# Kernel optimization log

Hardware: AMD Instinct MI355X
Metric: run time of the kernel (lower is better)

## Reference

```python
import jax, jax.numpy as jnp
import numpy as np

N, E = 50000, 800000
NFEAT, HID, NHEAD, NCLASS = 256, 32, 8, 40
NEG_SLOPE = 0.2


def gat_conv(x, src, dst, W, a_src, a_dst, bias, heads, out_ch, concat):
    n = x.shape[0]
    h = (x @ W).reshape(n, heads, out_ch)              # [N, H, C]
    alpha_src = jnp.einsum('nhc,hc->nh', h, a_src)     # [N, H]
    alpha_dst = jnp.einsum('nhc,hc->nh', h, a_dst)
    e = jax.nn.leaky_relu(alpha_src[src] + alpha_dst[dst], NEG_SLOPE)  # [E, H]
    # segment softmax over incoming edges of each dst node
    m = jax.ops.segment_max(e, dst, num_segments=n)
    ex = jnp.exp(e - m[dst])
    s = jax.ops.segment_sum(ex, dst, num_segments=n)
    alpha = ex / (s[dst] + 1e-16)                      # [E, H]
    out = jax.ops.segment_sum(h[src] * alpha[:, :, None], dst, num_segments=n)  # [N, H, C]
    out = out.reshape(n, heads * out_ch) if concat else out.mean(axis=1)
    return out + bias


def setup_inputs() -> dict:
    key = jax.random.key(0)
    ks = jax.random.split(key, 12)
    x = jax.random.normal(ks[0], (N, NFEAT), dtype=jnp.float32)
    edge_index = jax.random.randint(ks[1], (2, E), 0, N, dtype=jnp.int64)
    edge_attr = jax.random.normal(ks[2], (E, 8), dtype=jnp.float32)  # unused by the model
    s1 = 1.0 / np.sqrt(NFEAT)
    s2 = 1.0 / np.sqrt(HID * NHEAD)
    W1 = jax.random.normal(ks[3], (NFEAT, NHEAD * HID), dtype=jnp.float32) * s1
    att_src1 = jax.random.normal(ks[4], (NHEAD, HID), dtype=jnp.float32) * 0.1
    att_dst1 = jax.random.normal(ks[5], (NHEAD, HID), dtype=jnp.float32) * 0.1
    b1 = jnp.zeros((NHEAD * HID,), dtype=jnp.float32)
    W2 = jax.random.normal(ks[6], (NHEAD * HID, NCLASS), dtype=jnp.float32) * s2
    att_src2 = jax.random.normal(ks[7], (1, NCLASS), dtype=jnp.float32) * 0.1
    att_dst2 = jax.random.normal(ks[8], (1, NCLASS), dtype=jnp.float32) * 0.1
    b2 = jnp.zeros((NCLASS,), dtype=jnp.float32)
    return {"x": x, "edge_index": edge_index, "edge_attr": edge_attr,
            "W1": W1, "att_src1": att_src1, "att_dst1": att_dst1, "b1": b1,
            "W2": W2, "att_src2": att_src2, "att_dst2": att_dst2, "b2": b2}


def reference(x, edge_index, edge_attr, W1, att_src1, att_dst1, b1, W2, att_src2, att_dst2, b2):
    # eval mode: dropout is identity. GATConv adds self-loops by default.
    n = x.shape[0]
    loops = jnp.arange(n, dtype=edge_index.dtype)
    src = jnp.concatenate([edge_index[0], loops])
    dst = jnp.concatenate([edge_index[1], loops])
    h = jax.nn.elu(gat_conv(x, src, dst, W1, att_src1, att_dst1, b1, NHEAD, HID, True))
    final = gat_conv(h, src, dst, W2, att_src2, att_dst2, b2, 1, NCLASS, False)
    return final, jax.nn.log_softmax(final, axis=1)
```

## Files before the change

### kernel.cpp

```cpp
#include <hip/hip_runtime.h>
#include <hip/hip_bf16.h>
#include <hip/hip_fp16.h>
#include <math.h>

#define NN 50000
#define EE 800000
#define ET 850000
#define F1 256
#define NHEAD 8
#define HID 32
#define NCLASS 40
#define NEG 0.2f

typedef __attribute__((ext_vector_type(8))) short short8_t;
typedef __attribute__((ext_vector_type(4))) float float4_t;

__device__ __forceinline__ int clampN(int v) {
    return v < 0 ? 0 : (v >= NN ? NN - 1 : v);
}
__device__ __forceinline__ unsigned short f2bf(float f) {
    __hip_bfloat16 h = __float2bfloat16(f);
    return __builtin_bit_cast(unsigned short, h);
}
__device__ __forceinline__ float bf2f(unsigned short u) {
    return __uint_as_float((unsigned)u << 16);
}
__device__ __forceinline__ unsigned short f2h(float f) {
    __half h = __float2half(f);
    return __builtin_bit_cast(unsigned short, h);
}
__device__ __forceinline__ float h2f(unsigned short u) {
    __half h = __builtin_bit_cast(__half, u);
    return __half2float(h);
}
__device__ __forceinline__ float hlo2f(unsigned int u) {
    return h2f((unsigned short)(u & 0xFFFFu));
}
__device__ __forceinline__ float hhi2f(unsigned int u) {
    return h2f((unsigned short)(u >> 16));
}

__global__ __launch_bounds__(256) void hist_kernel(const int* __restrict__ ei, int* __restrict__ deg,
                                                   unsigned int* __restrict__ pack) {
    int t = blockIdx.x * 256 + threadIdx.x;
    if (t >= ET) return;
    int d = (t < EE) ? ei[EE + t] : (t - EE);
    d = clampN(d);
    int r = atomicAdd(&deg[d], 1);
    pack[t] = ((unsigned)d << 15) | (unsigned)r;
}

__global__ __launch_bounds__(256) void scan1_kernel(const int* __restrict__ deg, int* __restrict__ off, int* __restrict__ bsum) {
    __shared__ int lds[256];
    int b = blockIdx.x, tid = threadIdx.x;
    int base = b * 1024 + tid * 4;
    int v0 = (base + 0 < NN) ? deg[base + 0] : 0;
    int v1 = (base + 1 < NN) ? deg[base + 1] : 0;
    int v2 = (base + 2 < NN) ? deg[base + 2] : 0;
    int v3 = (base + 3 < NN) ? deg[base + 3] : 0;
    int s1 = v0 + v1, s2 = s1 + v2, s3 = s2 + v3;
    lds[tid] = s3;
    __syncthreads();
    for (int o = 1; o < 256; o <<= 1) {
        int t = (tid >= o) ? lds[tid - o] : 0;
        __syncthreads();
        if (tid >= o) lds[tid] += t;
        __syncthreads();
    }
    int excl = tid ? lds[tid - 1] : 0;
    if (base + 0 < NN) off[base + 1] = excl + v0;
    if (base + 1 < NN) off[base + 2] = excl + s1;
    if (base + 2 < NN) off[base + 3] = excl + s2;
    if (base + 3 < NN) off[base + 4] = excl + s3;
    if (tid == 255) bsum[b] = lds[255];
}

__global__ __launch_bounds__(256) void scan2_kernel(int* __restrict__ bsum, int nb) {
    __shared__ int lds[256];
    int tid = threadIdx.x;
    lds[tid] = (tid < nb) ? bsum[tid] : 0;
    __syncthreads();
    for (int o = 1; o < 256; o <<= 1) {
        int t = (tid >= o) ? lds[tid - o] : 0;
        __syncthreads();
        if (tid >= o) lds[tid] += t;
        __syncthreads();
    }
    if (tid < nb) bsum[tid] = lds[tid];
}

__global__ __launch_bounds__(256) void scan3_kernel(int* __restrict__ off, const int* __restrict__ bsum) {
    int b = blockIdx.x, tid = threadIdx.x;
    if (b == 0 && tid == 0) off[0] = 0;
    if (b == 0) return;
    int add = bsum[b - 1];
    int base = b * 1024 + tid * 4;
    #pragma unroll
    for (int i = 0; i < 4; ++i) {
        if (base + i < NN) off[base + i + 1] += add;
    }
}

__global__ __launch_bounds__(256) void scatter_kernel(const int* __restrict__ ei, const int* __restrict__ off,
                                                      const unsigned int* __restrict__ pack, int* __restrict__ esrc) {
    int t = blockIdx.x * 256 + threadIdx.x;
    if (t >= ET) return;
    unsigned p = pack[t];
    int d = p >> 15;
    int r = p & 0x7FFF;
    int s = (t < EE) ? ei[t] : (t - EE);
    s = clampN(s);
    esrc[off[d] + r] = s;
}

__global__ __launch_bounds__(256) void prep_kernel(const float* __restrict__ W1,
                                                   const float* __restrict__ as1, const float* __restrict__ ad1,
                                                   unsigned short* __restrict__ Bh, unsigned short* __restrict__ Bl) {
    int n = blockIdx.x;
    int k = threadIdx.x;
    float v;
    if (n < 256) {
        v = W1[(size_t)k * 256 + n];
    } else {
        int j = n - 256;
        int h = j & 7;
        const float* att = (j < 8) ? (as1 + h * 32) : (ad1 + h * 32);
        float s = 0.f;
        #pragma unroll
        for (int c = 0; c < 32; ++c) s += W1[(size_t)k * 256 + h * 32 + c] * att[c];
        v = s;
    }
    unsigned short hi = f2bf(v);
    Bh[n * 256 + k] = hi;
    Bl[n * 256 + k] = f2bf(v - bf2f(hi));
}

#define AKP 40
__global__ __launch_bounds__(256, 2) void gemm1_kernel(const float* __restrict__ x,
                                                       const unsigned short* __restrict__ Bh,
                                                       const unsigned short* __restrict__ Bl,
                                                       unsigned short* __restrict__ h1b,
                                                       float* __restrict__ asrc1, float* __restrict__ adst1) {
    __shared__ __align__(16) unsigned short Ah[128 * AKP];
    __shared__ __align__(16) unsigned short Al[128 * AKP];
    __shared__ __align__(16) unsigned short Bhs[272 * AKP];
    __shared__ __align__(16) unsigned short Bls[272 * AKP];
    int tid = threadIdx.x;
    int wave = tid >> 6, lane = tid & 63;
    int quad = lane >> 4, l16 = lane & 15;
    int row0 = blockIdx.x * 128;

    float4_t acc[2][17];
    #pragma unroll
    for (int i = 0; i < 2; ++i)
        #pragma unroll
        for (int j = 0; j < 17; ++j) acc[i][j] = (float4_t){0.f, 0.f, 0.f, 0.f};

    for (int k0 = 0; k0 < 256; k0 += 32) {
        __syncthreads();
        #pragma unroll
        for (int i = 0; i < 4; ++i) {
            int id = i * 256 + tid;
            int r = id >> 3, kq = id & 7;
            int rr = row0 + r; if (rr >= NN) rr = NN - 1;
            float4 v = *(const float4*)(x + (size_t)rr * 256 + k0 + kq * 4);
            ushort4 hi, lo;
            hi.x = f2bf(v.x); lo.x = f2bf(v.x - bf2f(hi.x));
            hi.y = f2bf(v.y); lo.y = f2bf(v.y - bf2f(hi.y));
            hi.z = f2bf(v.z); lo.z = f2bf(v.z - bf2f(hi.z));
            hi.w = f2bf(v.w); lo.w = f2bf(v.w - bf2f(hi.w));
            *(ushort4*)(Ah + r * AKP + kq * 4) = hi;
            *(ushort4*)(Al + r * AKP + kq * 4) = lo;
        }
        for (int id = tid; id < 272 * 4; id += 256) {
            int r = id >> 2, kq = id & 3;
            *(float4*)(Bhs + r * AKP + kq * 8) = *(const float4*)(Bh + (size_t)r * 256 + k0 + kq * 8);
            *(float4*)(Bls + r * AKP + kq * 8) = *(const float4*)(Bl + (size_t)r * 256 + k0 + kq * 8);
        }
        __syncthreads();
        short8_t ah[2], al[2];
        #pragma unroll
        for (int mt = 0; mt < 2; ++mt) {
            int mrow = wave * 32 + mt * 16 + l16;
            ah[mt] = *(const short8_t*)(Ah + mrow * AKP + quad * 8);
            al[mt] = *(const short8_t*)(Al + mrow * AKP + quad * 8);
        }
        #pragma unroll
        for (int nt = 0; nt < 17; ++nt) {
            int nrow = nt * 16 + l16;
            short8_t bh  = *(const short8_t*)(Bhs + nrow * AKP + quad * 8);
            short8_t blo = *(const short8_t*)(Bls + nrow * AKP + quad * 8);
            #pragma unroll
            for (int mt = 0; mt < 2; ++mt) {
                acc[mt][nt] = __builtin_amdgcn_mfma_f32_16x16x32_bf16(ah[mt], bh,  acc[mt][nt], 0, 0, 0);
                acc[mt][nt] = __builtin_amdgcn_mfma_f32_16x16x32_bf16(ah[mt], blo, acc[mt][nt], 0, 0, 0);
                acc[mt][nt] = __builtin_amdgcn_mfma_f32_16x16x32_bf16(al[mt], bh,  acc[mt][nt], 0, 0, 0);
            }
        }
    }
    #pragma unroll
    for (int mt = 0; mt < 2; ++mt) {
        int rbase = row0 + wave * 32 + mt * 16 + quad * 4;
        #pragma unroll
        for (int r = 0; r < 4; ++r) {
            int row = rbase + r;
            if (row >= NN) continue;
            #pragma unroll
            for (int nt = 0; nt < 16; ++nt)
                h1b[(size_t)row * 256 + nt * 16 + l16] = f2h(acc[mt][nt][r]);
            float v = acc[mt][16][r];
            if (l16 < 8) asrc1[row * 8 + l16] = v;
            else         adst1[row * 8 + (l16 - 8)] = v;
        }
    }
}

#define WST 68
__global__ __launch_bounds__(256) void agg1_kernel(const unsigned short* __restrict__ h1b, const float* __restrict__ asrc,
                                                   const float* __restrict__ adst, const int* __restrict__ esrc,
                                                   const int* __restrict__ off,
                                                   const float* __restrict__ b1, unsigned short* __restrict__ hout) {
    __shared__ __align__(16) float wl[4][8 * WST];
    __shared__ __align__(16) int  snl[4][64];
    int tid = threadIdx.x;
    int wave = tid >> 6;
    int wid = blockIdx.x * 4 + wave;
    if (wid >= NN) return;
    int lane = tid & 63;
    int hp = lane & 7;
    int jp = lane >> 3;
    int hc = lane >> 3;
    int c0 = lane * 4;
    float adh_p = adst[wid * 8 + hp];
    int e0 = off[wid], e1 = off[wid + 1];
    float* wlw = wl[wave];
    int* snw = snl[wave];
    const char* hb = (const char*)h1b;
    unsigned lofs = (unsigned)c0 * 2;

    float m = -INFINITY, s = 0.f;
    float ax = 0.f, ay = 0.f, az = 0.f, aw = 0.f;

    for (int base = e0; base < e1; base += 64) {
        int cnt = e1 - base; if (cnt > 64) cnt = 64;
        int snv = esrc[base + (lane < cnt ? lane : cnt - 1)];
        snw[lane] = snv;
        int nch = (cnt + 7) >> 3;
        float ee[8];
        float wmax = -INFINITY;
        #pragma unroll
        for (int cj = 0; cj < 8; ++cj) {
            if (cj >= nch) { ee[cj] = -INFINITY; continue; }
            int jedge = cj * 8 + jp;
            int sj = __shfl(snv, jedge);
            float a = asrc[sj * 8 + hp];
            float e = a + adh_p;
            e = (e >= 0.f) ? e : NEG * e;
            if (jedge >= cnt) e = -INFINITY;
            ee[cj] = e;
            wmax = fmaxf(wmax, e);
        }
        wmax = fmaxf(wmax, __shfl_xor(wmax, 8));
        wmax = fmaxf(wmax, __shfl_xor(wmax, 16));
        wmax = fmaxf(wmax, __shfl_xor(wmax, 32));
        float mn = fmaxf(m, wmax);
        float t = __expf(m - mn);
        m = mn;
        s *= t;
        float tc = __shfl(t, hc);
        ax *= tc; ay *= tc; az *= tc; aw *= tc;
        #pragma unroll
        for (int cj = 0; cj < 8; ++cj) {
            if (cj >= nch) break;
            float w = __expf(ee[cj] - mn);
            s += w;
            wlw[hp * WST + cj * 8 + jp] = w;
        }
        const float* wrow = wlw + hc * WST;
        for (int j = 0; j < cnt; j += 4) {
            float4 w4 = *(const float4*)(wrow + j);
            int4 sn4 = *(const int4*)(snw + j);
            uint2 u0 = *(const uint2*)(hb + (((unsigned)sn4.x << 9) + lofs));
            uint2 u1 = *(const uint2*)(hb + (((unsigned)sn4.y << 9) + lofs));
            uint2 u2 = *(const uint2*)(hb + (((unsigned)sn4.z << 9) + lofs));
            uint2 u3 = *(const uint2*)(hb + (((unsigned)sn4.w << 9) + lofs));
            ax += w4.x * hlo2f(u0.x);
            ay += w4.x * hhi2f(u0.x);
            az += w4.x * hlo2f(u0.y);
            aw += w4.x * hhi2f(u0.y);
            ax += w4.y * hlo2f(u1.x);
            ay += w4.y * hhi2f(u1.x);
            az += w4.y * hlo2f(u1.y);
            aw += w4.y * hhi2f(u1.y);
            ax += w4.z * hlo2f(u2.x);
            ay += w4.z * hhi2f(u2.x);
            az += w4.z * hlo2f(u2.y);
            aw += w4.z * hhi2f(u2.y);
            ax += w4.w * hlo2f(u3.x);
            ay += w4.w * hhi2f(u3.x);
            az += w4.w * hlo2f(u3.y);
            aw += w4.w * hhi2f(u3.y);
        }
    }
    s += __shfl_xor(s, 8);
    s += __shfl_xor(s, 16);
    s += __shfl_xor(s, 32);
    float sh = __shfl(s, hc);
    float inv = 1.f / (sh + 1e-16f);
    float4 b = *(const float4*)(b1 + c0);
    float vx = ax * inv + b.x, vy = ay * inv + b.y, vz = az * inv + b.z, vw = aw * inv + b.w;
    ushort4 o;
    o.x = f2h((vx > 0.f) ? vx : expm1f(vx));
    o.y = f2h((vy > 0.f) ? vy : expm1f(vy));
    o.z = f2h((vz > 0.f) ? vz : expm1f(vz));
    o.w = f2h((vw > 0.f) ? vw : expm1f(vw));
    *(ushort4*)(hout + (size_t)wid * 256 + c0) = o;
}

#define G2_TM 128
#define G2_KC 32
__global__ __launch_bounds__(256) void gemm2_kernel(const unsigned short* __restrict__ h, const float* __restrict__ W2,
                                                    const float* __restrict__ at_s, const float* __restrict__ at_d,
                                                    unsigned short* __restrict__ h2b, float* __restrict__ as2,
                                                    float* __restrict__ ad2) {
    __shared__ __align__(16) float w2s[256 * 40];
    __shared__ __align__(16) float As[G2_KC][132];
    int tid = threadIdx.x;
    for (int i = tid; i < 256 * 40; i += 256) w2s[i] = W2[i];
    int g  = tid & 7;
    int rg = tid >> 3;
    int row0 = blockIdx.x * G2_TM;
    float acc[4][5] = {};
    float ats[5], atd[5];
    #pragma unroll
    for (int j = 0; j < 5; ++j) { ats[j] = at_s[g + 8 * j]; atd[j] = at_d[g + 8 * j]; }

    for (int k0 = 0; k0 < 256; k0 += G2_KC) {
        __syncthreads();
        #pragma unroll
        for (int i = 0; i < 2; ++i) {
            int id = i * 256 + tid;
            int r  = id >> 2;
            int kq = id & 3;
            int rr = row0 + r; if (rr >= NN) rr = NN - 1;
            uint4 u = *(const uint4*)(h + (size_t)rr * 256 + k0 + kq * 8);
            As[kq * 8 + 0][r] = hlo2f(u.x);
            As[kq * 8 + 1][r] = hhi2f(u.x);
            As[kq * 8 + 2][r] = hlo2f(u.y);
            As[kq * 8 + 3][r] = hhi2f(u.y);
            As[kq * 8 + 4][r] = hlo2f(u.z);
            As[kq * 8 + 5][r] = hhi2f(u.z);
            As[kq * 8 + 6][r] = hlo2f(u.w);
            As[kq * 8 + 7][r] = hhi2f(u.w);
        }
        __syncthreads();
        #pragma unroll 4
        for (int k = 0; k < G2_KC; ++k) {
            float4 a = *(const float4*)(&As[k][rg * 4]);
            float w[5];
            #pragma unroll
            for (int j = 0; j < 5; ++j) w[j] = w2s[(k0 + k) * 40 + g + 8 * j];
            float av[4] = {a.x, a.y, a.z, a.w};
            #pragma unroll
            for (int r = 0; r < 4; ++r)
                #pragma unroll
                for (int j = 0; j < 5; ++j)
                    acc[r][j] += av[r] * w[j];
        }
    }

    #pragma unroll
    for (int r = 0; r < 4; ++r) {
        int row = row0 + rg * 4 + r;
        float ps = 0.f, pd = 0.f;
        #pragma unroll
        for (int j = 0; j < 5; ++j) {
            ps += acc[r][j] * ats[j];
            pd += acc[r][j] * atd[j];
        }
        ps += __shfl_xor(ps, 1); pd += __shfl_xor(pd, 1);
        ps += __shfl_xor(ps, 2); pd += __shfl_xor(pd, 2);
        ps += __shfl_xor(ps, 4); pd += __shfl_xor(pd, 4);
        if (row < NN) {
            #pragma unroll
            for (int j = 0; j < 5; ++j) h2b[(size_t)row * 40 + g + 8 * j] = f2h(acc[r][j]);
            if (g == 0) { as2[row] = ps; ad2[row] = pd; }
        }
    }
}

__global__ __launch_bounds__(256) void agg2_kernel(const unsigned short* __restrict__ h2b, const float* __restrict__ asrc,
                                                   const float* __restrict__ adst, const int* __restrict__ esrc,
                                                   const int* __restrict__ off,
                                                   const float* __restrict__ b2, float* __restrict__ outF,
                                                   float* __restrict__ outL) {
    __shared__ __align__(16) float wl2[4][64];
    __shared__ __align__(16) int  snl2[4][64];
    int tid = threadIdx.x;
    int wave = tid >> 6;
    int wid = blockIdx.x * 4 + wave;
    if (wid >= NN) return;
    int lane = tid & 63;
    int c = lane;
    float adh = adst[wid];
    int e0 = off[wid], e1 = off[wid + 1];
    const char* hb = (const char*)h2b + ((unsigned)(c < NCLASS ? c : 0) << 1);
    float* wlw = wl2[wave];
    int* snw = snl2[wave];

    float m = -INFINITY, s = 0.f, acc = 0.f;

    for (int base = e0; base < e1; base += 64) {
        int cnt = e1 - base; if (cnt > 64) cnt = 64;
        int snv = esrc[base + (lane < cnt ? lane : cnt - 1)];
        snw[lane] = snv;
        float a = asrc[snv];
        float e = a + adh;
        e = (e >= 0.f) ? e : NEG * e;
        if (lane >= cnt) e = -INFINITY;
        float cm = e;
        cm = fmaxf(cm, __shfl_xor(cm, 1));
        cm = fmaxf(cm, __shfl_xor(cm, 2));
        cm = fmaxf(cm, __shfl_xor(cm, 4));
        cm = fmaxf(cm, __shfl_xor(cm, 8));
        cm = fmaxf(cm, __shfl_xor(cm, 16));
        cm = fmaxf(cm, __shfl_xor(cm, 32));
        float mn = fmaxf(m, cm);
        float t = __expf(m - mn);
        float w = __expf(e - mn);
        s = s * t + w;
        m = mn;
        wlw[lane] = w;
        acc *= t;
        for (int j = 0; j < cnt; j += 4) {
            float4 w4 = *(const float4*)(wlw + j);
            int4 sn4 = *(const int4*)(snw + j);
            unsigned short v0 = *(const unsigned short*)(hb + (unsigned)sn4.x * 80);
            unsigned short v1 = *(const unsigned short*)(hb + (unsigned)sn4.y * 80);
            unsigned short v2 = *(const unsigned short*)(hb + (unsigned)sn4.z * 80);
            unsigned short v3 = *(const unsigned short*)(hb + (unsigned)sn4.w * 80);
            acc += w4.x * h2f(v0);
            acc += w4.y * h2f(v1);
            acc += w4.z * h2f(v2);
            acc += w4.w * h2f(v3);
        }
    }
    s += __shfl_xor(s, 1);
    s += __shfl_xor(s, 2);
    s += __shfl_xor(s, 4);
    s += __shfl_xor(s, 8);
    s += __shfl_xor(s, 16);
    s += __shfl_xor(s, 32);
    float inv = 1.f / (s + 1e-16f);
    float fin = (c < NCLASS) ? (acc * inv + b2[c]) : -INFINITY;
    if (c < NCLASS) outF[(size_t)wid * 40 + c] = fin;
    float mx = fin;
    for (int o = 32; o; o >>= 1) mx = fmaxf(mx, __shfl_xor(mx, o));
    float ex = (c < NCLASS) ? __expf(fin - mx) : 0.f;
    float sm = ex;
    for (int o = 32; o; o >>= 1) sm += __shfl_xor(sm, o);
    if (c < NCLASS) outL[(size_t)wid * 40 + c] = fin - mx - __logf(sm);
}

extern "C" void kernel_launch(void* const* d_in, const int* in_sizes, int n_in,
                              void* d_out, int out_size, void* d_ws, size_t ws_size,
                              hipStream_t stream) {
    const float* x   = (const float*)d_in[0];
    const int*   ei  = (const int*)d_in[1];
    const float* W1  = (const float*)d_in[3];
    const float* as1 = (const float*)d_in[4];
    const float* ad1 = (const float*)d_in[5];
    const float* b1  = (const float*)d_in[6];
    const float* W2  = (const float*)d_in[7];
    const float* as2c = (const float*)d_in[8];
    const float* ad2c = (const float*)d_in[9];
    const float* b2  = (const float*)d_in[10];

    float* outF = (float*)d_out;
    float* outL = outF + (size_t)NN * NCLASS;

    char* w = (char*)d_ws;
    auto alloc = [&](size_t bytes) {
        void* p = (void*)w;
        w += (bytes + 255) & ~(size_t)255;
        return p;
    };
    unsigned short* h1b = (unsigned short*)alloc((size_t)NN * 256 * 2);
    unsigned short* hbuf = (unsigned short*)alloc((size_t)NN * 256 * 2);
    unsigned short* h2b = (unsigned short*)alloc((size_t)NN * 40 * 2);
    float* asrc1 = (float*)alloc((size_t)NN * 8 * 4);
    float* adst1 = (float*)alloc((size_t)NN * 8 * 4);
    float* asrc2 = (float*)alloc((size_t)NN * 4);
    float* adst2 = (float*)alloc((size_t)NN * 4);
    int* deg    = (int*)alloc((size_t)NN * 4);
    int* off    = (int*)alloc((size_t)(NN + 1) * 4);
    unsigned int* pack = (unsigned int*)alloc((size_t)ET * 4);
    int* esrc   = (int*)alloc((size_t)ET * 4);
    int* bsum   = (int*)alloc(64 * 4);
    unsigned short* W1th = (unsigned short*)alloc((size_t)272 * 256 * 2);
    unsigned short* W1tl = (unsigned short*)alloc((size_t)272 * 256 * 2);

    const int NB_SCAN = (NN + 1023) / 1024;

    hipMemsetAsync(deg, 0, (size_t)NN * 4, stream);

    hist_kernel<<<(ET + 255) / 256, 256, 0, stream>>>(ei, deg, pack);
    scan1_kernel<<<NB_SCAN, 256, 0, stream>>>(deg, off, bsum);
    scan2_kernel<<<1, 256, 0, stream>>>(bsum, NB_SCAN);
    scan3_kernel<<<NB_SCAN, 256, 0, stream>>>(off, bsum);
    scatter_kernel<<<(ET + 255) / 256, 256, 0, stream>>>(ei, off, pack, esrc);

    prep_kernel<<<272, 256, 0, stream>>>(W1, as1, ad1, W1th, W1tl);
    gemm1_kernel<<<(NN + 127) / 128, 256, 0, stream>>>(x, W1th, W1tl, h1b, asrc1, adst1);
    agg1_kernel<<<(NN + 3) / 4, 256, 0, stream>>>(h1b, asrc1, adst1, esrc, off, b1, hbuf);
    gemm2_kernel<<<(NN + G2_TM - 1) / G2_TM, 256, 0, stream>>>(hbuf, W2, as2c, ad2c, h2b, asrc2, adst2);
    agg2_kernel<<<(NN + 3) / 4, 256, 0, stream>>>(h2b, asrc2, adst2, esrc, off, b2, outF, outL);
}
```

Before: 341.3 us.

## Use persistent grid-stride waves and scalar row addressing in GAT aggregation kernels

Both aggregation kernels now launch a fixed grid of 2048 blocks, and each wave loops over destination nodes with a grid stride instead of handling one node per wave. The gather loop is unrolled to 8 edges per step, and the source row indices are made wave-uniform with readfirstlane so addressing can use scalar registers. Edge slots are padded to multiples of 8, and the padded slots carry zero weights and repeat the last valid index. The aim is to cut launch and block-scheduling overhead and to put more loads in flight. The risk is load imbalance across waves and some wasted loads on padded edges.

Result: no change. 346.5 us (+1.5%).

```diff
diff --git a/kernel.cpp b/kernel.cpp
--- a/kernel.cpp
+++ b/kernel.cpp
@@ -224,97 +224,130 @@
     __shared__ __align__(16) int  snl[4][64];
     int tid = threadIdx.x;
     int wave = tid >> 6;
-    int wid = blockIdx.x * 4 + wave;
-    if (wid >= NN) return;
     int lane = tid & 63;
     int hp = lane & 7;
     int jp = lane >> 3;
     int hc = lane >> 3;
     int c0 = lane * 4;
-    float adh_p = adst[wid * 8 + hp];
-    int e0 = off[wid], e1 = off[wid + 1];
     float* wlw = wl[wave];
     int* snw = snl[wave];
+    const float* wrow = wlw + hc * WST;
     const char* hb = (const char*)h1b;
     unsigned lofs = (unsigned)c0 * 2;
-
-    float m = -INFINITY, s = 0.f;
-    float ax = 0.f, ay = 0.f, az = 0.f, aw = 0.f;
-
-    for (int base = e0; base < e1; base += 64) {
-        int cnt = e1 - base; if (cnt > 64) cnt = 64;
-        int snv = esrc[base + (lane < cnt ? lane : cnt - 1)];
-        snw[lane] = snv;
-        int nch = (cnt + 7) >> 3;
-        float ee[8];
-        float wmax = -INFINITY;
-        #pragma unroll
-        for (int cj = 0; cj < 8; ++cj) {
-            if (cj >= nch) { ee[cj] = -INFINITY; continue; }
-            int jedge = cj * 8 + jp;
-            int sj = __shfl(snv, jedge);
-            float a = asrc[sj * 8 + hp];
-            float e = a + adh_p;
-            e = (e >= 0.f) ? e : NEG * e;
-            if (jedge >= cnt) e = -INFINITY;
-            ee[cj] = e;
-            wmax = fmaxf(wmax, e);
-        }
-        wmax = fmaxf(wmax, __shfl_xor(wmax, 8));
-        wmax = fmaxf(wmax, __shfl_xor(wmax, 16));
-        wmax = fmaxf(wmax, __shfl_xor(wmax, 32));
-        float mn = fmaxf(m, wmax);
-        float t = __expf(m - mn);
-        m = mn;
-        s *= t;
-        float tc = __shfl(t, hc);
-        ax *= tc; ay *= tc; az *= tc; aw *= tc;
-        #pragma unroll
-        for (int cj = 0; cj < 8; ++cj) {
-            if (cj >= nch) break;
-            float w = __expf(ee[cj] - mn);
-            s += w;
-            wlw[hp * WST + cj * 8 + jp] = w;
-        }
-        const float* wrow = wlw + hc * WST;
-        for (int j = 0; j < cnt; j += 4) {
-            float4 w4 = *(const float4*)(wrow + j);
-            int4 sn4 = *(const int4*)(snw + j);
-            uint2 u0 = *(const uint2*)(hb + (((unsigned)sn4.x << 9) + lofs));
-            uint2 u1 = *(const uint2*)(hb + (((unsigned)sn4.y << 9) + lofs));
-            uint2 u2 = *(const uint2*)(hb + (((unsigned)sn4.z << 9) + lofs));
-            uint2 u3 = *(const uint2*)(hb + (((unsigned)sn4.w << 9) + lofs));
-            ax += w4.x * hlo2f(u0.x);
-            ay += w4.x * hhi2f(u0.x);
-            az += w4.x * hlo2f(u0.y);
-            aw += w4.x * hhi2f(u0.y);
-            ax += w4.y * hlo2f(u1.x);
-            ay += w4.y * hhi2f(u1.x);
-            az += w4.y * hlo2f(u1.y);
-            aw += w4.y * hhi2f(u1.y);
-            ax += w4.z * hlo2f(u2.x);
-            ay += w4.z * hhi2f(u2.x);
-            az += w4.z * hlo2f(u2.y);
-            aw += w4.z * hhi2f(u2.y);
-            ax += w4.w * hlo2f(u3.x);
-            ay += w4.w * hhi2f(u3.x);
-            az += w4.w * hlo2f(u3.y);
-            aw += w4.w * hhi2f(u3.y);
-        }
-    }
-    s += __shfl_xor(s, 8);
-    s += __shfl_xor(s, 16);
-    s += __shfl_xor(s, 32);
-    float sh = __shfl(s, hc);
-    float inv = 1.f / (sh + 1e-16f);
     float4 b = *(const float4*)(b1 + c0);
-    float vx = ax * inv + b.x, vy = ay * inv + b.y, vz = az * inv + b.z, vw = aw * inv + b.w;
-    ushort4 o;
-    o.x = f2h((vx > 0.f) ? vx : expm1f(vx));
-    o.y = f2h((vy > 0.f) ? vy : expm1f(vy));
-    o.z = f2h((vz > 0.f) ? vz : expm1f(vz));
-    o.w = f2h((vw > 0.f) ? vw : expm1f(vw));
-    *(ushort4*)(hout + (size_t)wid * 256 + c0) = o;
+    int wstride = gridDim.x * 4;
+
+    for (int wid = blockIdx.x * 4 + wave; wid < NN; wid += wstride) {
+        float adh_p = adst[wid * 8 + hp];
+        int e0 = off[wid], e1 = off[wid + 1];
+
+        float m = -INFINITY, s = 0.f;
+        float ax = 0.f, ay = 0.f, az = 0.f, aw = 0.f;
+
+        for (int base = e0; base < e1; base += 64) {
+            int cnt = e1 - base; if (cnt > 64) cnt = 64;
+            int snv = esrc[base + (lane < cnt ? lane : cnt - 1)];
+            snw[lane] = snv;
+            int nch = (cnt + 7) >> 3;
+            float ee[8];
+            float wmax = -INFINITY;
+            #pragma unroll
+            for (int cj = 0; cj < 8; ++cj) {
+                if (cj >= nch) { ee[cj] = -INFINITY; continue; }
+                int jedge = cj * 8 + jp;
+                int sj = __shfl(snv, jedge);
+                float a = asrc[sj * 8 + hp];
+                float e = a + adh_p;
+                e = (e >= 0.f) ? e : NEG * e;
+                if (jedge >= cnt) e = -INFINITY;
+                ee[cj] = e;
+                wmax = fmaxf(wmax, e);
+            }
+            wmax = fmaxf(wmax, __shfl_xor(wmax, 8));
+            wmax = fmaxf(wmax, __shfl_xor(wmax, 16));
+            wmax = fmaxf(wmax, __shfl_xor(wmax, 32));
+            float mn = fmaxf(m, wmax);
+            float t = __expf(m - mn);
+            m = mn;
+            s *= t;
+            float tc = __shfl(t, hc);
+            ax *= tc; ay *= tc; az *= tc; aw *= tc;
+            #pragma unroll
+            for (int cj = 0; cj < 8; ++cj) {
+                if (cj >= nch) break;
+                float w = __expf(ee[cj] - mn);
+                s += w;
+                wlw[hp * WST + cj * 8 + jp] = w;
+            }
+            int nslots = nch * 8;
+            for (int j = 0; j < nslots; j += 8) {
+                float4 wa = *(const float4*)(wrow + j);
+                float4 wb = *(const float4*)(wrow + j + 4);
+                int4 sa = *(const int4*)(snw + j);
+                int4 sb = *(const int4*)(snw + j + 4);
+                const char* r0 = hb + ((size_t)(unsigned)__builtin_amdgcn_readfirstlane(sa.x) << 9);
+                const char* r1 = hb + ((size_t)(unsigned)__builtin_amdgcn_readfirstlane(sa.y) << 9);
+                const char* r2 = hb + ((size_t)(unsigned)__builtin_amdgcn_readfirstlane(sa.z) << 9);
+                const char* r3 = hb + ((size_t)(unsigned)__builtin_amdgcn_readfirstlane(sa.w) << 9);
+                const char* r4 = hb + ((size_t)(unsigned)__builtin_amdgcn_readfirstlane(sb.x) << 9);
+                const char* r5 = hb + ((size_t)(unsigned)__builtin_amdgcn_readfirstlane(sb.y) << 9);
+                const char* r6 = hb + ((size_t)(unsigned)__builtin_amdgcn_readfirstlane(sb.z) << 9);
+                const char* r7 = hb + ((size_t)(unsigned)__builtin_amdgcn_readfirstlane(sb.w) << 9);
+                uint2 u0 = *(const uint2*)(r0 + lofs);
+                uint2 u1 = *(const uint2*)(r1 + lofs);
+                uint2 u2 = *(const uint2*)(r2 + lofs);
+                uint2 u3 = *(const uint2*)(r3 + lofs);
+                uint2 u4 = *(const uint2*)(r4 + lofs);
+                uint2 u5 = *(const uint2*)(r5 + lofs);
+                uint2 u6 = *(const uint2*)(r6 + lofs);
+                uint2 u7 = *(const uint2*)(r7 + lofs);
+                ax += wa.x * hlo2f(u0.x);
+                ay += wa.x * hhi2f(u0.x);
+                az += wa.x * hlo2f(u0.y);
+                aw += wa.x * hhi2f(u0.y);
+                ax += wa.y * hlo2f(u1.x);
+                ay += wa.y * hhi2f(u1.x);
+                az += wa.y * hlo2f(u1.y);
+                aw += wa.y * hhi2f(u1.y);
+                ax += wa.z * hlo2f(u2.x);
+                ay += wa.z * hhi2f(u2.x);
+                az += wa.z * hlo2f(u2.y);
+                aw += wa.z * hhi2f(u2.y);
+                ax += wa.w * hlo2f(u3.x);
+                ay += wa.w * hhi2f(u3.x);
+                az += wa.w * hlo2f(u3.y);
+                aw += wa.w * hhi2f(u3.y);
+                ax += wb.x * hlo2f(u4.x);
+                ay += wb.x * hhi2f(u4.x);
+                az += wb.x * hlo2f(u4.y);
+                aw += wb.x * hhi2f(u4.y);
+                ax += wb.y * hlo2f(u5.x);
+                ay += wb.y * hhi2f(u5.x);
+                az += wb.y * hlo2f(u5.y);
+                aw += wb.y * hhi2f(u5.y);
+                ax += wb.z * hlo2f(u6.x);
+                ay += wb.z * hhi2f(u6.x);
+                az += wb.z * hlo2f(u6.y);
+                aw += wb.z * hhi2f(u6.y);
+                ax += wb.w * hlo2f(u7.x);
+                ay += wb.w * hhi2f(u7.x);
+                az += wb.w * hlo2f(u7.y);
+                aw += wb.w * hhi2f(u7.y);
+            }
+        }
+        s += __shfl_xor(s, 8);
+        s += __shfl_xor(s, 16);
+        s += __shfl_xor(s, 32);
+        float sh = __shfl(s, hc);
+        float inv = 1.f / (sh + 1e-16f);
+        float vx = ax * inv + b.x, vy = ay * inv + b.y, vz = az * inv + b.z, vw = aw * inv + b.w;
+        ushort4 o;
+        o.x = f2h((vx > 0.f) ? vx : expm1f(vx));
+        o.y = f2h((vy > 0.f) ? vy : expm1f(vy));
+        o.z = f2h((vz > 0.f) ? vz : expm1f(vz));
+        o.w = f2h((vw > 0.f) ? vw : expm1f(vw));
+        *(ushort4*)(hout + (size_t)wid * 256 + c0) = o;
+    }
 }
 
 #define G2_TM 128
@@ -398,68 +431,91 @@
     __shared__ __align__(16) int  snl2[4][64];
     int tid = threadIdx.x;
     int wave = tid >> 6;
-    int wid = blockIdx.x * 4 + wave;
-    if (wid >= NN) return;
     int lane = tid & 63;
     int c = lane;
-    float adh = adst[wid];
-    int e0 = off[wid], e1 = off[wid + 1];
-    const char* hb = (const char*)h2b + ((unsigned)(c < NCLASS ? c : 0) << 1);
+    const char* hb = (const char*)h2b;
+    unsigned coff = (unsigned)(c < NCLASS ? c : 0) * 2;
     float* wlw = wl2[wave];
     int* snw = snl2[wave];
-
-    float m = -INFINITY, s = 0.f, acc = 0.f;
-
-    for (int base = e0; base < e1; base += 64) {
-        int cnt = e1 - base; if (cnt > 64) cnt = 64;
-        int snv = esrc[base + (lane < cnt ? lane : cnt - 1)];
-        snw[lane] = snv;
-        float a = asrc[snv];
-        float e = a + adh;
-        e = (e >= 0.f) ? e : NEG * e;
-        if (lane >= cnt) e = -INFINITY;
-        float cm = e;
-        cm = fmaxf(cm, __shfl_xor(cm, 1));
-        cm = fmaxf(cm, __shfl_xor(cm, 2));
-        cm = fmaxf(cm, __shfl_xor(cm, 4));
-        cm = fmaxf(cm, __shfl_xor(cm, 8));
-        cm = fmaxf(cm, __shfl_xor(cm, 16));
-        cm = fmaxf(cm, __shfl_xor(cm, 32));
-        float mn = fmaxf(m, cm);
-        float t = __expf(m - mn);
-        float w = __expf(e - mn);
-        s = s * t + w;
-        m = mn;
-        wlw[lane] = w;
-        acc *= t;
-        for (int j = 0; j < cnt; j += 4) {
-            float4 w4 = *(const float4*)(wlw + j);
-            int4 sn4 = *(const int4*)(snw + j);
-            unsigned short v0 = *(const unsigned short*)(hb + (unsigned)sn4.x * 80);
-            unsigned short v1 = *(const unsigned short*)(hb + (unsigned)sn4.y * 80);
-            unsigned short v2 = *(const unsigned short*)(hb + (unsigned)sn4.z * 80);
-            unsigned short v3 = *(const unsigned short*)(hb + (unsigned)sn4.w * 80);
-            acc += w4.x * h2f(v0);
-            acc += w4.y * h2f(v1);
-            acc += w4.z * h2f(v2);
-            acc += w4.w * h2f(v3);
-        }
-    }
-    s += __shfl_xor(s, 1);
-    s += __shfl_xor(s, 2);
-    s += __shfl_xor(s, 4);
-    s += __shfl_xor(s, 8);
-    s += __shfl_xor(s, 16);
-    s += __shfl_xor(s, 32);
-    float inv = 1.f / (s + 1e-16f);
-    float fin = (c < NCLASS) ? (acc * inv + b2[c]) : -INFINITY;
-    if (c < NCLASS) outF[(size_t)wid * 40 + c] = fin;
-    float mx = fin;
-    for (int o = 32; o; o >>= 1) mx = fmaxf(mx, __shfl_xor(mx, o));
-    float ex = (c < NCLASS) ? __expf(fin - mx) : 0.f;
-    float sm = ex;
-    for (int o = 32; o; o >>= 1) sm += __shfl_xor(sm, o);
-    if (c < NCLASS) outL[(size_t)wid * 40 + c] = fin - mx - __logf(sm);
+    float bc = (c < NCLASS) ? b2[c] : 0.f;
+    int wstride = gridDim.x * 4;
+
+    for (int wid = blockIdx.x * 4 + wave; wid < NN; wid += wstride) {
+        float adh = adst[wid];
+        int e0 = off[wid], e1 = off[wid + 1];
+
+        float m = -INFINITY, s = 0.f, acc = 0.f;
+
+        for (int base = e0; base < e1; base += 64) {
+            int cnt = e1 - base; if (cnt > 64) cnt = 64;
+            int snv = esrc[base + (lane < cnt ? lane : cnt - 1)];
+            snw[lane] = snv;
+            float a = asrc[snv];
+            float e = a + adh;
+            e = (e >= 0.f) ? e : NEG * e;
+            if (lane >= cnt) e = -INFINITY;
+            float cm = e;
+            cm = fmaxf(cm, __shfl_xor(cm, 1));
+            cm = fmaxf(cm, __shfl_xor(cm, 2));
+            cm = fmaxf(cm, __shfl_xor(cm, 4));
+            cm = fmaxf(cm, __shfl_xor(cm, 8));
+            cm = fmaxf(cm, __shfl_xor(cm, 16));
+            cm = fmaxf(cm, __shfl_xor(cm, 32));
+            float mn = fmaxf(m, cm);
+            float t = __expf(m - mn);
+            float w = __expf(e - mn);
+            s = s * t + w;
+            m = mn;
+            wlw[lane] = w;
+            acc *= t;
+            int n8 = (cnt + 7) & ~7;
+            for (int j = 0; j < n8; j += 8) {
+                float4 wa = *(const float4*)(wlw + j);
+                float4 wb = *(const float4*)(wlw + j + 4);
+                int4 sa = *(const int4*)(snw + j);
+                int4 sb = *(const int4*)(snw + j + 4);
+                const char* r0 = hb + (size_t)((unsigned)__builtin_amdgcn_readfirstlane(sa.x) * 80u);
+                const char* r1 = hb + (size_t)((unsigned)__builtin_amdgcn_readfirstlane(sa.y) * 80u);
+                const char* r2 = hb + (size_t)((unsigned)__builtin_amdgcn_readfirstlane(sa.z) * 80u);
+                const char* r3 = hb + (size_t)((unsigned)__builtin_amdgcn_readfirstlane(sa.w) * 80u);
+                const char* r4 = hb + (size_t)((unsigned)__builtin_amdgcn_readfirstlane(sb.x) * 80u);
+                const char* r5 = hb + (size_t)((unsigned)__builtin_amdgcn_readfirstlane(sb.y) * 80u);
+                const char* r6 = hb + (size_t)((unsigned)__builtin_amdgcn_readfirstlane(sb.z) * 80u);
+                const char* r7 = hb + (size_t)((unsigned)__builtin_amdgcn_readfirstlane(sb.w) * 80u);
+                unsigned short v0 = *(const unsigned short*)(r0 + coff);
+                unsigned short v1 = *(const unsigned short*)(r1 + coff);
+                unsigned short v2 = *(const unsigned short*)(r2 + coff);
+                unsigned short v3 = *(const unsigned short*)(r3 + coff);
+                unsigned short v4 = *(const unsigned short*)(r4 + coff);
+                unsigned short v5 = *(const unsigned short*)(r5 + coff);
+                unsigned short v6 = *(const unsigned short*)(r6 + coff);
+                unsigned short v7 = *(const unsigned short*)(r7 + coff);
+                acc += wa.x * h2f(v0);
+                acc += wa.y * h2f(v1);
+                acc += wa.z * h2f(v2);
+                acc += wa.w * h2f(v3);
+                acc += wb.x * h2f(v4);
+                acc += wb.y * h2f(v5);
+                acc += wb.z * h2f(v6);
+                acc += wb.w * h2f(v7);
+            }
+        }
+        s += __shfl_xor(s, 1);
+        s += __shfl_xor(s, 2);
+        s += __shfl_xor(s, 4);
+        s += __shfl_xor(s, 8);
+        s += __shfl_xor(s, 16);
+        s += __shfl_xor(s, 32);
+        float inv = 1.f / (s + 1e-16f);
+        float fin = (c < NCLASS) ? (acc * inv + bc) : -INFINITY;
+        if (c < NCLASS) outF[(size_t)wid * 40 + c] = fin;
+        float mx = fin;
+        for (int o = 32; o; o >>= 1) mx = fmaxf(mx, __shfl_xor(mx, o));
+        float ex = (c < NCLASS) ? __expf(fin - mx) : 0.f;
+        float sm = ex;
+        for (int o = 32; o; o >>= 1) sm += __shfl_xor(sm, o);
+        if (c < NCLASS) outL[(size_t)wid * 40 + c] = fin - mx - __logf(sm);
+    }
 }
 
 extern "C" void kernel_launch(void* const* d_in, const int* in_sizes, int n_in,
@@ -512,7 +568,7 @@
 
     prep_kernel<<<272, 256, 0, stream>>>(W1, as1, ad1, W1th, W1tl);
     gemm1_kernel<<<(NN + 127) / 128, 256, 0, stream>>>(x, W1th, W1tl, h1b, asrc1, adst1);
-    agg1_kernel<<<(NN + 3) / 4, 256, 0, stream>>>(h1b, asrc1, adst1, esrc, off, b1, hbuf);
+    agg1_kernel<<<2048, 256, 0, stream>>>(h1b, asrc1, adst1, esrc, off, b1, hbuf);
     gemm2_kernel<<<(NN + G2_TM - 1) / G2_TM, 256, 0, stream>>>(hbuf, W2, as2c, ad2c, h2b, asrc2, adst2);
-    agg2_kernel<<<(NN + 3) / 4, 256, 0, stream>>>(h2b, asrc2, adst2, esrc, off, b2, outF, outL);
-}
+    agg2_kernel<<<2048, 256, 0, stream>>>(h2b, asrc2, adst2, esrc, off, b2, outF, outL);
+}
```
